# Optimization experiments

Hardware: AMD Instinct MI355X
Metric: run time of the kernel (lower is better)

Reference implementation:

```python
import jax, jax.numpy as jnp
import numpy as np

FP8_MAX = 448.0  # max finite value of float8_e4m3fn


def setup_inputs() -> dict:
    key = jax.random.key(0)
    k1, k2, k3 = jax.random.split(key, 3)
    T, H = 8192, 4096
    x = jax.random.normal(k1, (T, H), dtype=jnp.float32)
    w = jax.random.uniform(k2, (H, H), dtype=jnp.float32)  # stored as fp8 in the module; quantized in reference
    wscale = jax.random.uniform(k3, (1,), dtype=jnp.float32)
    return {"x": x, "w": w, "wscale": wscale}


def reference(x, w, wscale):
    # Dynamic per-token activation quantization to fp8 e4m3 (symmetric).
    x_scale = jnp.max(jnp.abs(x), axis=-1, keepdims=True) / FP8_MAX  # [T, 1]
    x_scale = jnp.maximum(x_scale, jnp.float32(1e-12))
    x_q = jnp.clip(x / x_scale, -FP8_MAX, FP8_MAX).astype(jnp.float8_e4m3fn)
    # Weight is stored in fp8 (per-tensor scale wscale); replicate the cast.
    w_q = w.astype(jnp.float8_e4m3fn)
    # Scaled fp8 matmul with fp32 accumulation, then dequant by x_scale * wscale.
    y = jnp.einsum('tk,kh->th', x_q.astype(jnp.float32), w_q.astype(jnp.float32))
    y = y * x_scale * wscale  # [T, H]
    # tensor_model_parallel_all_reduce is identity on a single device.
    return y
```

## Files before the change

### kernel.cpp

```cpp
#include <hip/hip_runtime.h>
#include <stdint.h>

#define T_DIM 8192
#define K_DIM 4096
#define N_DIM 4096
#define FP8MAX 448.0f

typedef __attribute__((ext_vector_type(4))) float floatx4;
typedef __attribute__((ext_vector_type(4))) int   intx4;
typedef __attribute__((ext_vector_type(8))) int   intx8;


__device__ static inline void load16_g2lds(const void* gptr, void* lptr) {
    __builtin_amdgcn_global_load_lds(
        (const __attribute__((address_space(1))) void*)gptr,
        (__attribute__((address_space(3))) void*)lptr,
        16, 0, 0);
}

__device__ static inline uint32_t pack4_fp8(float f0, float f1, float f2, float f3) {
    int p = 0;
    p = __builtin_amdgcn_cvt_pk_fp8_f32(f0, f1, p, false);
    p = __builtin_amdgcn_cvt_pk_fp8_f32(f2, f3, p, true);
    return (uint32_t)p;
}

__global__ __launch_bounds__(256) void quant_fused_kernel(
    const float* __restrict__ x, const float* __restrict__ w,
    uint8_t* __restrict__ xq, uint8_t* __restrict__ wqT,
    float* __restrict__ xscale)
{
    const int tid = threadIdx.x;
    if (blockIdx.x < T_DIM) {
        const int t = blockIdx.x;
        const int lane = tid & 63;
        const int wave = tid >> 6;
        const float4* xr4 = (const float4*)(x + (size_t)t * K_DIM);

        float4 v[4];
        float m = 0.0f;
#pragma unroll
        for (int e = 0; e < 4; ++e) {
            v[e] = xr4[tid + e * 256];
            m = fmaxf(m, fmaxf(fmaxf(fabsf(v[e].x), fabsf(v[e].y)),
                               fmaxf(fabsf(v[e].z), fabsf(v[e].w))));
        }
#pragma unroll
        for (int off = 32; off > 0; off >>= 1)
            m = fmaxf(m, __shfl_down(m, off, 64));
        __shared__ float red[4];
        if (lane == 0) red[wave] = m;
        __syncthreads();
        float mm = fmaxf(fmaxf(red[0], red[1]), fmaxf(red[2], red[3]));
        float scale = fmaxf(mm / FP8MAX, 1e-12f);
        if (tid == 0) xscale[t] = scale;
        const float inv = 1.0f / scale;

        uint32_t* xqr = (uint32_t*)(xq + (size_t)t * K_DIM);
#pragma unroll
        for (int e = 0; e < 4; ++e) {
            float q0 = fminf(fmaxf(v[e].x * inv, -FP8MAX), FP8MAX);
            float q1 = fminf(fmaxf(v[e].y * inv, -FP8MAX), FP8MAX);
            float q2 = fminf(fmaxf(v[e].z * inv, -FP8MAX), FP8MAX);
            float q3 = fminf(fmaxf(v[e].w * inv, -FP8MAX), FP8MAX);
            xqr[tid + e * 256] = pack4_fp8(q0, q1, q2, q3);
        }
    } else {
        const int b = blockIdx.x - T_DIM;
        const int n0 = (b & 63) * 64;
        const int k0 = (b >> 6) * 64;
        __shared__ uint32_t tile[64][17];

#pragma unroll
        for (int e = 0; e < 4; ++e) {
            int idx = tid + e * 256;
            int r = idx >> 4;
            int c4 = idx & 15;
            float4 v = *(const float4*)(w + (size_t)(k0 + r) * N_DIM + n0 + c4 * 4);
            tile[r][c4] = pack4_fp8(v.x, v.y, v.z, v.w);
        }
        __syncthreads();
        const int kg = tid & 15;
        const int ng = tid >> 4;
        uint32_t in0 = tile[kg * 4 + 0][ng];
        uint32_t in1 = tile[kg * 4 + 1][ng];
        uint32_t in2 = tile[kg * 4 + 2][ng];
        uint32_t in3 = tile[kg * 4 + 3][ng];
#pragma unroll
        for (int i = 0; i < 4; ++i) {
            uint32_t o = ((in0 >> (8 * i)) & 0xFFu)
                       | (((in1 >> (8 * i)) & 0xFFu) << 8)
                       | (((in2 >> (8 * i)) & 0xFFu) << 16)
                       | (((in3 >> (8 * i)) & 0xFFu) << 24);
            *(uint32_t*)(wqT + (size_t)(n0 + ng * 4 + i) * K_DIM + k0 + kg * 4) = o;
        }
    }
}

__global__ __launch_bounds__(256, 3) void gemm_fp8_kernel(
    const uint8_t* __restrict__ xq, const uint8_t* __restrict__ wqT,
    const float* __restrict__ xscale, const float* __restrict__ wscale,
    float* __restrict__ out)
{
    __shared__ __align__(16) uint8_t As[128 * 128];
    __shared__ __align__(16) uint8_t Bs[128 * 128];

    const int tid = threadIdx.x;
    const int lane = tid & 63;
    const int wave = tid >> 6;
    const int m0 = blockIdx.y * 128;
    const int n0 = blockIdx.x * 128;
    const int wm = (wave >> 1) * 64;
    const int wn = (wave & 1) * 64;
    const int row = lane & 15;
    const int quad = lane >> 4;

    floatx4 acc[4][4] = {{{0.f,0.f,0.f,0.f}}};

    const uint8_t* gA[4];
    const uint8_t* gB[4];
    uint8_t* lA[4];
    uint8_t* lB[4];
#pragma unroll
    for (int p = 0; p < 4; ++p) {
        const int c = tid + p * 256;
        const int r = c >> 3, gg = c & 7, g = gg ^ (r & 7);
        gA[p] = xq  + (size_t)(m0 + r) * K_DIM + g * 16;
        gB[p] = wqT + (size_t)(n0 + r) * K_DIM + g * 16;
        lA[p] = As + c * 16;
        lB[p] = Bs + c * 16;
    }

    int aoff0[4], aoff1[4], boff0[4], boff1[4];
#pragma unroll
    for (int i = 0; i < 4; ++i) {
        const int mr = wm + i * 16 + row;
        const int nr = wn + i * 16 + row;
        aoff0[i] = mr * 128 + (((2 * quad)     ^ (mr & 7)) << 4);
        aoff1[i] = mr * 128 + (((2 * quad + 1) ^ (mr & 7)) << 4);
        boff0[i] = nr * 128 + (((2 * quad)     ^ (nr & 7)) << 4);
        boff1[i] = nr * 128 + (((2 * quad + 1) ^ (nr & 7)) << 4);
    }

    for (int k0 = 0; k0 < K_DIM; k0 += 128) {
        __syncthreads();
#pragma unroll
        for (int p = 0; p < 4; ++p) {
            load16_g2lds(gA[p] + k0, lA[p]);
            load16_g2lds(gB[p] + k0, lB[p]);
        }
        __syncthreads();

        intx8 a[4], b[4];
#pragma unroll
        for (int i = 0; i < 4; ++i) {
            intx4 lo = *(const intx4*)(As + aoff0[i]);
            intx4 hi = *(const intx4*)(As + aoff1[i]);
            a[i] = __builtin_shufflevector(lo, hi, 0, 1, 2, 3, 4, 5, 6, 7);
        }
#pragma unroll
        for (int j = 0; j < 4; ++j) {
            intx4 lo = *(const intx4*)(Bs + boff0[j]);
            intx4 hi = *(const intx4*)(Bs + boff1[j]);
            b[j] = __builtin_shufflevector(lo, hi, 0, 1, 2, 3, 4, 5, 6, 7);
        }
#pragma unroll
        for (int i = 0; i < 4; ++i)
#pragma unroll
            for (int j = 0; j < 4; ++j)
                acc[i][j] = __builtin_amdgcn_mfma_scale_f32_16x16x128_f8f6f4(
                    a[i], b[j], acc[i][j],
                    0, 0,
                    0, 0x7F7F7F7F,
                    0, 0x7F7F7F7F);
    }

    const float wsv = wscale[0];
#pragma unroll
    for (int i = 0; i < 4; ++i) {
        const int rbase = m0 + wm + i * 16 + quad * 4;
        float s[4];
#pragma unroll
        for (int r = 0; r < 4; ++r) s[r] = xscale[rbase + r] * wsv;
#pragma unroll
        for (int j = 0; j < 4; ++j) {
            const int col = n0 + wn + j * 16 + row;
#pragma unroll
            for (int r = 0; r < 4; ++r)
                out[(size_t)(rbase + r) * N_DIM + col] = acc[i][j][r] * s[r];
        }
    }
}


extern "C" void kernel_launch(void* const* d_in, const int* in_sizes, int n_in,
                              void* d_out, int out_size, void* d_ws, size_t ws_size,
                              hipStream_t stream) {
    const float* x      = (const float*)d_in[0];
    const float* w      = (const float*)d_in[1];
    const float* wscale = (const float*)d_in[2];
    float* out = (float*)d_out;

    uint8_t* xq  = (uint8_t*)d_ws;
    uint8_t* wqT = xq + (size_t)T_DIM * K_DIM;
    float* xscale = (float*)(wqT + (size_t)N_DIM * K_DIM);

    quant_fused_kernel<<<T_DIM + (N_DIM / 64) * (K_DIM / 64), 256, 0, stream>>>(
        x, w, xq, wqT, xscale);
    gemm_fp8_kernel<<<dim3(N_DIM / 128, T_DIM / 128), 256, 0, stream>>>(
        xq, wqT, xscale, wscale, out);
}
```

Measured before the change: 389.0 us.

## Triple-buffer LDS with interleaved async loads and 256x128 GEMM tiles

Turns the FP8 GEMM into a 512-thread, 256x128 tile kernel with a three-stage LDS ring buffer. Global-to-LDS loads for the tile two steps ahead are spread between the MFMA row groups, using manual vmcnt waits, s_barrier and s_setprio to overlap memory with matrix math. It also adds a grouped block-index swizzle to improve L2 reuse, and each B tile is shared by twice as many rows. The cost is 144KB of LDS per block, which limits occupancy, plus many more barriers per iteration.

```diff
diff --git a/kernel.cpp b/kernel.cpp
--- a/kernel.cpp
+++ b/kernel.cpp
@@ -5,6 +5,8 @@
 #define K_DIM 4096
 #define N_DIM 4096
 #define FP8MAX 448.0f
+#define NT     32
+#define BUFB   49152
 
 typedef __attribute__((ext_vector_type(4))) float floatx4;
 typedef __attribute__((ext_vector_type(4))) int   intx4;
@@ -97,38 +99,44 @@
     }
 }
 
-__global__ __launch_bounds__(256, 3) void gemm_fp8_kernel(
+__global__ __launch_bounds__(512, 2) void gemm_fp8_kernel(
     const uint8_t* __restrict__ xq, const uint8_t* __restrict__ wqT,
     const float* __restrict__ xscale, const float* __restrict__ wscale,
     float* __restrict__ out)
 {
-    __shared__ __align__(16) uint8_t As[128 * 128];
-    __shared__ __align__(16) uint8_t Bs[128 * 128];
-
-    const int tid = threadIdx.x;
+    __shared__ __align__(16) uint8_t lds[3 * BUFB];
+
+    const int tid  = threadIdx.x;
     const int lane = tid & 63;
     const int wave = tid >> 6;
-    const int m0 = blockIdx.y * 128;
-    const int n0 = blockIdx.x * 128;
+
+    const int bid = blockIdx.y * gridDim.x + blockIdx.x;
+    const int swz = (bid & 7) * 128 + (bid >> 3);
+    const int m0 = (swz >> 5) * 256;
+    const int n0 = (swz & 31) * 128;
+
     const int wm = (wave >> 1) * 64;
     const int wn = (wave & 1) * 64;
-    const int row = lane & 15;
+    const int row  = lane & 15;
     const int quad = lane >> 4;
 
     floatx4 acc[4][4] = {{{0.f,0.f,0.f,0.f}}};
 
-    const uint8_t* gA[4];
-    const uint8_t* gB[4];
-    uint8_t* lA[4];
-    uint8_t* lB[4];
+    const uint8_t* gA[4]; uint32_t lA[4];
+    const uint8_t* gB[2]; uint32_t lB[2];
 #pragma unroll
     for (int p = 0; p < 4; ++p) {
-        const int c = tid + p * 256;
+        const int c = tid + p * 512;
         const int r = c >> 3, gg = c & 7, g = gg ^ (r & 7);
-        gA[p] = xq  + (size_t)(m0 + r) * K_DIM + g * 16;
+        gA[p] = xq + (size_t)(m0 + r) * K_DIM + g * 16;
+        lA[p] = (uint32_t)c * 16u;
+    }
+#pragma unroll
+    for (int p = 0; p < 2; ++p) {
+        const int c = tid + p * 512;
+        const int r = c >> 3, gg = c & 7, g = gg ^ (r & 7);
         gB[p] = wqT + (size_t)(n0 + r) * K_DIM + g * 16;
-        lA[p] = As + c * 16;
-        lB[p] = Bs + c * 16;
+        lB[p] = 32768u + (uint32_t)c * 16u;
     }
 
     int aoff0[4], aoff1[4], boff0[4], boff1[4];
@@ -138,41 +146,90 @@
         const int nr = wn + i * 16 + row;
         aoff0[i] = mr * 128 + (((2 * quad)     ^ (mr & 7)) << 4);
         aoff1[i] = mr * 128 + (((2 * quad + 1) ^ (mr & 7)) << 4);
-        boff0[i] = nr * 128 + (((2 * quad)     ^ (nr & 7)) << 4);
-        boff1[i] = nr * 128 + (((2 * quad + 1) ^ (nr & 7)) << 4);
-    }
-
-    for (int k0 = 0; k0 < K_DIM; k0 += 128) {
-        __syncthreads();
-#pragma unroll
-        for (int p = 0; p < 4; ++p) {
-            load16_g2lds(gA[p] + k0, lA[p]);
-            load16_g2lds(gB[p] + k0, lB[p]);
-        }
-        __syncthreads();
+        boff0[i] = 32768 + nr * 128 + (((2 * quad)     ^ (nr & 7)) << 4);
+        boff1[i] = 32768 + nr * 128 + (((2 * quad + 1) ^ (nr & 7)) << 4);
+    }
+
+#define READ_A(i) { \
+    intx4 lo = *(const intx4*)(Ab + aoff0[i]); \
+    intx4 hi = *(const intx4*)(Ab + aoff1[i]); \
+    a[i] = __builtin_shufflevector(lo, hi, 0, 1, 2, 3, 4, 5, 6, 7); }
+#define READ_B(j) { \
+    intx4 lo = *(const intx4*)(Ab + boff0[j]); \
+    intx4 hi = *(const intx4*)(Ab + boff1[j]); \
+    b[j] = __builtin_shufflevector(lo, hi, 0, 1, 2, 3, 4, 5, 6, 7); }
+#define MFMA_ROW(i) \
+    acc[i][0] = __builtin_amdgcn_mfma_scale_f32_16x16x128_f8f6f4(a[i], b[0], acc[i][0], 0, 0, 0, 0x7F7F7F7F, 0, 0x7F7F7F7F); \
+    acc[i][1] = __builtin_amdgcn_mfma_scale_f32_16x16x128_f8f6f4(a[i], b[1], acc[i][1], 0, 0, 0, 0x7F7F7F7F, 0, 0x7F7F7F7F); \
+    acc[i][2] = __builtin_amdgcn_mfma_scale_f32_16x16x128_f8f6f4(a[i], b[2], acc[i][2], 0, 0, 0, 0x7F7F7F7F, 0, 0x7F7F7F7F); \
+    acc[i][3] = __builtin_amdgcn_mfma_scale_f32_16x16x128_f8f6f4(a[i], b[3], acc[i][3], 0, 0, 0, 0x7F7F7F7F, 0, 0x7F7F7F7F);
+
+#pragma unroll
+    for (int p = 0; p < 4; ++p) load16_g2lds(gA[p], &lds[lA[p]]);
+#pragma unroll
+    for (int p = 0; p < 2; ++p) load16_g2lds(gB[p], &lds[lB[p]]);
+#pragma unroll
+    for (int p = 0; p < 4; ++p) load16_g2lds(gA[p] + 128, &lds[BUFB + lA[p]]);
+#pragma unroll
+    for (int p = 0; p < 2; ++p) load16_g2lds(gB[p] + 128, &lds[BUFB + lB[p]]);
+
+    int rd = 0;
+    for (int t = 0; t < NT - 1; ++t) {
+        asm volatile("s_waitcnt vmcnt(6)" ::: "memory");
+        __builtin_amdgcn_s_barrier();
+        asm volatile("" ::: "memory");
+
+        const uint8_t* Ab = &lds[(uint32_t)rd * BUFB];
+        int st = rd + 2; if (st >= 3) st -= 3;
+        const uint32_t sb = (uint32_t)st * BUFB;
+        const int kk = (t + 2) * 128;
+        const bool stg = (t < NT - 2);
 
         intx8 a[4], b[4];
-#pragma unroll
-        for (int i = 0; i < 4; ++i) {
-            intx4 lo = *(const intx4*)(As + aoff0[i]);
-            intx4 hi = *(const intx4*)(As + aoff1[i]);
-            a[i] = __builtin_shufflevector(lo, hi, 0, 1, 2, 3, 4, 5, 6, 7);
-        }
-#pragma unroll
-        for (int j = 0; j < 4; ++j) {
-            intx4 lo = *(const intx4*)(Bs + boff0[j]);
-            intx4 hi = *(const intx4*)(Bs + boff1[j]);
-            b[j] = __builtin_shufflevector(lo, hi, 0, 1, 2, 3, 4, 5, 6, 7);
-        }
-#pragma unroll
-        for (int i = 0; i < 4; ++i)
-#pragma unroll
-            for (int j = 0; j < 4; ++j)
-                acc[i][j] = __builtin_amdgcn_mfma_scale_f32_16x16x128_f8f6f4(
-                    a[i], b[j], acc[i][j],
-                    0, 0,
-                    0, 0x7F7F7F7F,
-                    0, 0x7F7F7F7F);
+        READ_B(0); READ_B(1); READ_B(2); READ_B(3); READ_A(0);
+        if (stg) { load16_g2lds(gA[0] + kk, &lds[sb + lA[0]]);
+                   load16_g2lds(gA[1] + kk, &lds[sb + lA[1]]); }
+        __builtin_amdgcn_s_barrier();
+        __builtin_amdgcn_s_setprio(1);
+        MFMA_ROW(0);
+        __builtin_amdgcn_s_setprio(0);
+        __builtin_amdgcn_s_barrier();
+        READ_A(1);
+        if (stg) { load16_g2lds(gA[2] + kk, &lds[sb + lA[2]]);
+                   load16_g2lds(gA[3] + kk, &lds[sb + lA[3]]); }
+        __builtin_amdgcn_s_barrier();
+        __builtin_amdgcn_s_setprio(1);
+        MFMA_ROW(1);
+        __builtin_amdgcn_s_setprio(0);
+        __builtin_amdgcn_s_barrier();
+        READ_A(2);
+        if (stg) { load16_g2lds(gB[0] + kk, &lds[sb + lB[0]]);
+                   load16_g2lds(gB[1] + kk, &lds[sb + lB[1]]); }
+        __builtin_amdgcn_s_barrier();
+        __builtin_amdgcn_s_setprio(1);
+        MFMA_ROW(2);
+        __builtin_amdgcn_s_setprio(0);
+        __builtin_amdgcn_s_barrier();
+        READ_A(3);
+        __builtin_amdgcn_s_barrier();
+        __builtin_amdgcn_s_setprio(1);
+        MFMA_ROW(3);
+        __builtin_amdgcn_s_setprio(0);
+
+        rd = (rd == 2) ? 0 : rd + 1;
+    }
+
+    {
+        asm volatile("s_waitcnt vmcnt(0)" ::: "memory");
+        __builtin_amdgcn_s_barrier();
+        asm volatile("" ::: "memory");
+        const uint8_t* Ab = &lds[(uint32_t)rd * BUFB];
+        intx8 a[4], b[4];
+        READ_B(0); READ_B(1); READ_B(2); READ_B(3);
+        READ_A(0); MFMA_ROW(0);
+        READ_A(1); MFMA_ROW(1);
+        READ_A(2); MFMA_ROW(2);
+        READ_A(3); MFMA_ROW(3);
     }
 
     const float wsv = wscale[0];
@@ -190,6 +247,9 @@
                 out[(size_t)(rbase + r) * N_DIM + col] = acc[i][j][r] * s[r];
         }
     }
+#undef READ_A
+#undef READ_B
+#undef MFMA_ROW
 }
 
 
@@ -207,6 +267,6 @@
 
     quant_fused_kernel<<<T_DIM + (N_DIM / 64) * (K_DIM / 64), 256, 0, stream>>>(
         x, w, xq, wqT, xscale);
-    gemm_fp8_kernel<<<dim3(N_DIM / 128, T_DIM / 128), 256, 0, stream>>>(
+    gemm_fp8_kernel<<<dim3(N_DIM / 128, T_DIM / 256), 512, 0, stream>>>(
         xq, wqT, xscale, wscale, out);
 }
```

New measurement: 414.4 us. +6.5%, slower.

## Double-buffer LDS tiles in fp8 GEMM to overlap global loads with MFMA

Applied to the files above, without the earlier changes.

Allocates two 32KB LDS buffers and prefetches the next K-tile via global_load_lds while the current tile is read and fed to MFMAs. This removes one barrier per iteration and is meant to hide global-memory latency behind compute. It also raises wave priority around the MFMA block with s_setprio. LDS per block doubles to 64KB, which may lower occupancy below the launch-bound target of 3 blocks per CU.

```diff
diff --git a/kernel.cpp b/kernel.cpp
--- a/kernel.cpp
+++ b/kernel.cpp
@@ -5,6 +5,8 @@
 #define K_DIM 4096
 #define N_DIM 4096
 #define FP8MAX 448.0f
+#define NT     32
+#define BUFB   32768u
 
 typedef __attribute__((ext_vector_type(4))) float floatx4;
 typedef __attribute__((ext_vector_type(4))) int   intx4;
@@ -102,33 +104,31 @@
     const float* __restrict__ xscale, const float* __restrict__ wscale,
     float* __restrict__ out)
 {
-    __shared__ __align__(16) uint8_t As[128 * 128];
-    __shared__ __align__(16) uint8_t Bs[128 * 128];
-
-    const int tid = threadIdx.x;
+    __shared__ __align__(16) uint8_t lds[2 * BUFB];
+
+    const int tid  = threadIdx.x;
     const int lane = tid & 63;
     const int wave = tid >> 6;
     const int m0 = blockIdx.y * 128;
     const int n0 = blockIdx.x * 128;
     const int wm = (wave >> 1) * 64;
     const int wn = (wave & 1) * 64;
-    const int row = lane & 15;
+    const int row  = lane & 15;
     const int quad = lane >> 4;
 
     floatx4 acc[4][4] = {{{0.f,0.f,0.f,0.f}}};
 
     const uint8_t* gA[4];
     const uint8_t* gB[4];
-    uint8_t* lA[4];
-    uint8_t* lB[4];
+    uint32_t lA[4], lB[4];
 #pragma unroll
     for (int p = 0; p < 4; ++p) {
         const int c = tid + p * 256;
         const int r = c >> 3, gg = c & 7, g = gg ^ (r & 7);
         gA[p] = xq  + (size_t)(m0 + r) * K_DIM + g * 16;
         gB[p] = wqT + (size_t)(n0 + r) * K_DIM + g * 16;
-        lA[p] = As + c * 16;
-        lB[p] = Bs + c * 16;
+        lA[p] = (uint32_t)c * 16u;
+        lB[p] = 16384u + (uint32_t)c * 16u;
     }
 
     int aoff0[4], aoff1[4], boff0[4], boff1[4];
@@ -138,41 +138,51 @@
         const int nr = wn + i * 16 + row;
         aoff0[i] = mr * 128 + (((2 * quad)     ^ (mr & 7)) << 4);
         aoff1[i] = mr * 128 + (((2 * quad + 1) ^ (mr & 7)) << 4);
-        boff0[i] = nr * 128 + (((2 * quad)     ^ (nr & 7)) << 4);
-        boff1[i] = nr * 128 + (((2 * quad + 1) ^ (nr & 7)) << 4);
-    }
-
-    for (int k0 = 0; k0 < K_DIM; k0 += 128) {
+        boff0[i] = 16384 + nr * 128 + (((2 * quad)     ^ (nr & 7)) << 4);
+        boff1[i] = 16384 + nr * 128 + (((2 * quad + 1) ^ (nr & 7)) << 4);
+    }
+
+#define READ_A(i) { \
+    intx4 lo = *(const intx4*)(Ab + aoff0[i]); \
+    intx4 hi = *(const intx4*)(Ab + aoff1[i]); \
+    a[i] = __builtin_shufflevector(lo, hi, 0, 1, 2, 3, 4, 5, 6, 7); }
+#define READ_B(j) { \
+    intx4 lo = *(const intx4*)(Ab + boff0[j]); \
+    intx4 hi = *(const intx4*)(Ab + boff1[j]); \
+    b[j] = __builtin_shufflevector(lo, hi, 0, 1, 2, 3, 4, 5, 6, 7); }
+#define MFMA_ROW(i) \
+    acc[i][0] = __builtin_amdgcn_mfma_scale_f32_16x16x128_f8f6f4(a[i], b[0], acc[i][0], 0, 0, 0, 0x7F7F7F7F, 0, 0x7F7F7F7F); \
+    acc[i][1] = __builtin_amdgcn_mfma_scale_f32_16x16x128_f8f6f4(a[i], b[1], acc[i][1], 0, 0, 0, 0x7F7F7F7F, 0, 0x7F7F7F7F); \
+    acc[i][2] = __builtin_amdgcn_mfma_scale_f32_16x16x128_f8f6f4(a[i], b[2], acc[i][2], 0, 0, 0, 0x7F7F7F7F, 0, 0x7F7F7F7F); \
+    acc[i][3] = __builtin_amdgcn_mfma_scale_f32_16x16x128_f8f6f4(a[i], b[3], acc[i][3], 0, 0, 0, 0x7F7F7F7F, 0, 0x7F7F7F7F);
+
+#pragma unroll
+    for (int p = 0; p < 4; ++p) {
+        load16_g2lds(gA[p], &lds[lA[p]]);
+        load16_g2lds(gB[p], &lds[lB[p]]);
+    }
+    __syncthreads();
+
+    for (int t = 0; t < NT; ++t) {
+        if (t < NT - 1) {
+            const uint32_t nb = (uint32_t)((t + 1) & 1) * BUFB;
+            const int kk = (t + 1) * 128;
+#pragma unroll
+            for (int p = 0; p < 4; ++p) {
+                load16_g2lds(gA[p] + kk, &lds[nb + lA[p]]);
+                load16_g2lds(gB[p] + kk, &lds[nb + lB[p]]);
+            }
+        }
+
+        const uint8_t* Ab = &lds[(uint32_t)(t & 1) * BUFB];
+        intx8 a[4], b[4];
+        READ_A(0); READ_A(1); READ_A(2); READ_A(3);
+        READ_B(0); READ_B(1); READ_B(2); READ_B(3);
+        __builtin_amdgcn_s_setprio(1);
+        MFMA_ROW(0); MFMA_ROW(1); MFMA_ROW(2); MFMA_ROW(3);
+        __builtin_amdgcn_s_setprio(0);
+
         __syncthreads();
-#pragma unroll
-        for (int p = 0; p < 4; ++p) {
-            load16_g2lds(gA[p] + k0, lA[p]);
-            load16_g2lds(gB[p] + k0, lB[p]);
-        }
-        __syncthreads();
-
-        intx8 a[4], b[4];
-#pragma unroll
-        for (int i = 0; i < 4; ++i) {
-            intx4 lo = *(const intx4*)(As + aoff0[i]);
-            intx4 hi = *(const intx4*)(As + aoff1[i]);
-            a[i] = __builtin_shufflevector(lo, hi, 0, 1, 2, 3, 4, 5, 6, 7);
-        }
-#pragma unroll
-        for (int j = 0; j < 4; ++j) {
-            intx4 lo = *(const intx4*)(Bs + boff0[j]);
-            intx4 hi = *(const intx4*)(Bs + boff1[j]);
-            b[j] = __builtin_shufflevector(lo, hi, 0, 1, 2, 3, 4, 5, 6, 7);
-        }
-#pragma unroll
-        for (int i = 0; i < 4; ++i)
-#pragma unroll
-            for (int j = 0; j < 4; ++j)
-                acc[i][j] = __builtin_amdgcn_mfma_scale_f32_16x16x128_f8f6f4(
-                    a[i], b[j], acc[i][j],
-                    0, 0,
-                    0, 0x7F7F7F7F,
-                    0, 0x7F7F7F7F);
     }
 
     const float wsv = wscale[0];
@@ -190,6 +200,9 @@
                 out[(size_t)(rbase + r) * N_DIM + col] = acc[i][j][r] * s[r];
         }
     }
+#undef READ_A
+#undef READ_B
+#undef MFMA_ROW
 }
 
 
```

Measured after the change: 395.6 us. Within noise of the previous version (+1.7%).
